# Kernel optimization log

Hardware: AMD Instinct MI355X
Metric: run time of the kernel (lower is better)

## Reference

```python
import jax, jax.numpy as jnp
import numpy as np

GROUPS = 16
GROUP_SIZE = 16
K = 3
KK = K * K
BN_EPS = 1e-5


def setup_inputs() -> dict:
    key = jax.random.key(0)
    ks = jax.random.split(key, 6)
    B, C, H, W = 16, 256, 56, 56
    mid = C // 4  # rd_ratio = 4
    x = jax.random.normal(ks[0], (B, C, H, W), dtype=jnp.float32)
    w1 = jax.random.normal(ks[1], (mid, C), dtype=jnp.float32) * (1.0 / np.sqrt(C))
    bn_gamma = jnp.ones((mid,), dtype=jnp.float32)
    bn_beta = jnp.zeros((mid,), dtype=jnp.float32)
    bn_mean = jax.random.normal(ks[2], (mid,), dtype=jnp.float32) * 0.1
    bn_var = jax.random.uniform(ks[3], (mid,), dtype=jnp.float32, minval=0.5, maxval=1.5)
    w2 = jax.random.normal(ks[4], (KK * GROUPS, mid), dtype=jnp.float32) * (1.0 / np.sqrt(mid))
    b2 = jax.random.normal(ks[5], (KK * GROUPS,), dtype=jnp.float32) * 0.01
    return {"x": x, "w1": w1, "bn_gamma": bn_gamma, "bn_beta": bn_beta,
            "bn_mean": bn_mean, "bn_var": bn_var, "w2": w2, "b2": b2}


def reference(x, w1, bn_gamma, bn_beta, bn_mean, bn_var, w2, b2):
    B, C, H, W = x.shape
    # conv1: 1x1 conv + BatchNorm (eval) + ReLU
    t = jnp.einsum('bchw,oc->bohw', x, w1)
    scale = bn_gamma / jnp.sqrt(bn_var + BN_EPS)
    t = t * scale[None, :, None, None] + (bn_beta - bn_mean * scale)[None, :, None, None]
    t = jax.nn.relu(t)
    # conv2: 1x1 conv producing per-pixel kernels (B, KK*groups, H, W)
    weight = jnp.einsum('bchw,oc->bohw', t, w2) + b2[None, :, None, None]
    weight = weight.reshape(B, GROUPS, 1, KK, H, W)
    # unfold: extract 3x3 patches (pad=1, stride=1), kernel positions row-major
    xp = jnp.pad(x, ((0, 0), (0, 0), (1, 1), (1, 1)))
    patches = jnp.stack(
        [xp[:, :, i:i + H, j:j + W] for i in range(K) for j in range(K)],
        axis=2)  # (B, C, KK, H, W), matches torch unfold's (c*KK + kk) layout
    patches = patches.reshape(B, GROUPS, GROUP_SIZE, KK, H, W)
    out = (weight * patches).sum(axis=3).reshape(B, C, H, W)
    return out
```

## Files before the change

### kernel.cpp

```cpp
#include <hip/hip_runtime.h>


#define Cn    256
#define MID   64
#define Hn    56
#define Wn    56
#define HW    3136
#define Bn    16
#define NPIX  (Bn * HW)
#define CHW   (Cn * HW)
#define NKK   9
#define NG    16
#define GSZ   16
#define PXT   64
#define BN_EPS 1e-5f

#define GLOAD_LDS(src, dst, sz)                                                        \
  __builtin_amdgcn_global_load_lds(                                                    \
      (const __attribute__((address_space(1))) void*)(src),                            \
      (__attribute__((address_space(3))) void*)(dst), (sz), 0, 0)

__global__ __launch_bounds__(256) void prep_kernel(
    const float* __restrict__ w1,
    const float* __restrict__ gamma,
    const float* __restrict__ beta,
    const float* __restrict__ mean,
    const float* __restrict__ var,
    float* __restrict__ w1f,
    float* __restrict__ bias1) {
  int idx = blockIdx.x * 256 + threadIdx.x;
  if (idx < MID * Cn) {
    int c = idx >> 6;
    int o = idx & 63;
    float scale = gamma[o] / sqrtf(var[o] + BN_EPS);
    w1f[idx] = w1[o * Cn + c] * scale;
  } else if (idx < MID * Cn + MID) {
    int o = idx - MID * Cn;
    float scale = gamma[o] / sqrtf(var[o] + BN_EPS);
    bias1[o] = beta[o] - mean[o] * scale;
  }
}

__global__ __launch_bounds__(256) void conv1_kernel(
    const float* __restrict__ x,
    const float* __restrict__ w1f,
    const float* __restrict__ bias1,
    float* __restrict__ t) {
  __shared__ __align__(16) float lx[2][16][PXT];

  const int tid = threadIdx.x;
  const int px  = tid & 63;
  const int wv  = __builtin_amdgcn_readfirstlane(tid >> 6);

  const int bid = blockIdx.x;
  const int pc  = bid >> 1;
  const int oh  = bid & 1;
  const int px0 = pc * PXT;
  const int b   = px0 / HW;
  const int hw0 = px0 - b * HW;
  const float* xb = x + (size_t)b * CHW + hw0;

  const int rsub = px >> 4;
  const int csub = (px & 15) << 2;

  GLOAD_LDS(xb + (size_t)((wv << 2) + rsub) * HW + csub, &lx[0][wv << 2][0], 16);
  __syncthreads();

  float acc[8];
#pragma unroll
  for (int j = 0; j < 8; ++j) acc[j] = 0.0f;

  for (int k = 0; k < 16; ++k) {
    const int cur = k & 1;
    if (k < 15) {
      GLOAD_LDS(xb + (size_t)((k + 1) * 16 + (wv << 2) + rsub) * HW + csub,
                &lx[cur ^ 1][wv << 2][0], 16);
    }
#pragma unroll
    for (int c = 0; c < 16; ++c) {
      const float xv = lx[cur][c][px];
      const float* wr = w1f + (((k << 4) + c) << 6) + (oh << 5) + (wv << 3);
      const float4 wa = *(const float4*)(wr + 0);
      const float4 wb = *(const float4*)(wr + 4);
      acc[0] = fmaf(xv, wa.x, acc[0]);
      acc[1] = fmaf(xv, wa.y, acc[1]);
      acc[2] = fmaf(xv, wa.z, acc[2]);
      acc[3] = fmaf(xv, wa.w, acc[3]);
      acc[4] = fmaf(xv, wb.x, acc[4]);
      acc[5] = fmaf(xv, wb.y, acc[5]);
      acc[6] = fmaf(xv, wb.z, acc[6]);
      acc[7] = fmaf(xv, wb.w, acc[7]);
    }
    __syncthreads();
  }

#pragma unroll
  for (int j = 0; j < 8; ++j) {
    const int o = (oh << 5) + (wv << 3) + j;
    t[(size_t)o * NPIX + px0 + px] = fmaxf(acc[j] + bias1[o], 0.0f);
  }
}

__global__ __launch_bounds__(256) void conv2_inv_kernel(
    const float* __restrict__ x,
    const float* __restrict__ t,
    const float* __restrict__ w2,
    const float* __restrict__ b2,
    float* __restrict__ out) {
  __shared__ __align__(16) float lt[MID][PXT];

  const int tid = threadIdx.x;
  const int px  = tid & 63;
  const int wv  = __builtin_amdgcn_readfirstlane(tid >> 6);

  const int bid = blockIdx.x;
  const int pc  = bid >> 2;
  const int gq  = bid & 3;
  const int g   = (gq << 2) + wv;

  const int px0 = pc * PXT;
  const int b   = px0 / HW;
  const int hw0 = px0 - b * HW;

  const int rsub = px >> 4;
  const int csub = (px & 15) << 2;

#pragma unroll
  for (int j = 0; j < 4; ++j) {
    const int r0 = (wv << 4) + (j << 2);
    GLOAD_LDS(t + (size_t)(r0 + rsub) * NPIX + px0 + csub, &lt[r0][0], 16);
  }
  __syncthreads();

  float a[NKK];
#pragma unroll
  for (int kk = 0; kk < NKK; ++kk) a[kk] = b2[g * NKK + kk];

  const float* wg = w2 + (size_t)g * (NKK * MID);
#pragma unroll 4
  for (int o4 = 0; o4 < MID; o4 += 4) {
    const float t0 = lt[o4 + 0][px];
    const float t1 = lt[o4 + 1][px];
    const float t2 = lt[o4 + 2][px];
    const float t3 = lt[o4 + 3][px];
#pragma unroll
    for (int kk = 0; kk < NKK; ++kk) {
      const float4 w4 = *(const float4*)(wg + (kk << 6) + o4);
      a[kk] = fmaf(t3, w4.w, fmaf(t2, w4.z, fmaf(t1, w4.y, fmaf(t0, w4.x, a[kk]))));
    }
  }

  const int hw = hw0 + px;
  const int h  = hw / Wn;
  const int w  = hw - h * Wn;

  int off[NKK];
  unsigned vmask = 0;
#pragma unroll
  for (int kk = 0; kk < NKK; ++kk) {
    const int di  = kk / 3 - 1;
    const int dj  = kk % 3 - 1;
    const int h2  = h + di;
    const int w2v = w + dj;
    const bool valid = ((unsigned)h2 < (unsigned)Hn) && ((unsigned)w2v < (unsigned)Wn);
    off[kk] = valid ? (h2 * Wn + w2v) : hw;
    vmask |= (valid ? 1u : 0u) << kk;
  }

  float wk[NKK];
#pragma unroll
  for (int kk = 0; kk < NKK; ++kk)
    wk[kk] = ((vmask >> kk) & 1u) ? a[kk] : 0.0f;

  const float* xc = x + (size_t)b * CHW + (size_t)(g * GSZ) * HW;
  float* ob = out + (size_t)b * CHW + (size_t)(g * GSZ) * HW + hw;
#pragma unroll 4
  for (int cc = 0; cc < GSZ; ++cc) {
    const float* xp = xc + (size_t)cc * HW;
    float s0 = wk[0] * xp[off[0]];
    float s1 = wk[1] * xp[off[1]];
    float s2 = wk[2] * xp[off[2]];
    s0 = fmaf(wk[3], xp[off[3]], s0);
    s1 = fmaf(wk[4], xp[off[4]], s1);
    s2 = fmaf(wk[5], xp[off[5]], s2);
    s0 = fmaf(wk[6], xp[off[6]], s0);
    s1 = fmaf(wk[7], xp[off[7]], s1);
    s2 = fmaf(wk[8], xp[off[8]], s2);
    ob[(size_t)cc * HW] = s0 + s1 + s2;
  }
}

extern "C" void kernel_launch(void* const* d_in, const int* in_sizes, int n_in,
                              void* d_out, int out_size, void* d_ws, size_t ws_size,
                              hipStream_t stream) {
  const float* x     = (const float*)d_in[0];
  const float* w1    = (const float*)d_in[1];
  const float* gamma = (const float*)d_in[2];
  const float* beta  = (const float*)d_in[3];
  const float* mean  = (const float*)d_in[4];
  const float* var   = (const float*)d_in[5];
  const float* w2    = (const float*)d_in[6];
  const float* b2    = (const float*)d_in[7];
  float* out = (float*)d_out;

  char* ws = (char*)d_ws;
  float* t     = (float*)ws;
  float* w1f   = (float*)(ws + (size_t)MID * NPIX * 4);
  float* bias1 = (float*)(ws + (size_t)MID * NPIX * 4 + (size_t)MID * Cn * 4);

  prep_kernel<<<(MID * Cn + MID + 255) / 256, 256, 0, stream>>>(
      w1, gamma, beta, mean, var, w1f, bias1);
  conv1_kernel<<<NPIX / PXT * 2, 256, 0, stream>>>(x, w1f, bias1, t);
  conv2_inv_kernel<<<NPIX / PXT * 4, 256, 0, stream>>>(x, t, w2, b2, out);
}
```

Before: 161.9 us.

## Remap conv1 to lane-per-output-channel with LDS transpose; prefetch unfold loads in conv2

conv1 now assigns one output channel per lane and 16 pixels per wave. x values are read as wave-uniform broadcast loads and w1f per lane. Results are transposed through padded LDS so t is written with float4 stores, and the grid is halved since each block covers all 64 channels. conv2 issues the first four channels' 3x3 neighbor loads before the t barrier and the conv2 matmul. It then software-pipelines the remaining channel loads against compute, reorders the block index so group quads of neighboring pixel chunks run together, and sets a minimum occupancy bound. This adds register pressure and replaces LDS-staged x in conv1 with many scalar or broadcast global loads.

Result: slower. 183.2 us (+13.1%).

```diff
diff --git a/kernel.cpp b/kernel.cpp
--- a/kernel.cpp
+++ b/kernel.cpp
@@ -46,62 +46,80 @@
     const float* __restrict__ w1f,
     const float* __restrict__ bias1,
     float* __restrict__ t) {
-  __shared__ __align__(16) float lx[2][16][PXT];
-
-  const int tid = threadIdx.x;
-  const int px  = tid & 63;
-  const int wv  = __builtin_amdgcn_readfirstlane(tid >> 6);
+  __shared__ float lt2[PXT][MID + 1];
+
+  const int tid  = threadIdx.x;
+  const int lane = tid & 63;
+  const int wv   = __builtin_amdgcn_readfirstlane(tid >> 6);
 
   const int bid = blockIdx.x;
-  const int pc  = bid >> 1;
-  const int oh  = bid & 1;
-  const int px0 = pc * PXT;
-  const int b   = px0 / HW;
-  const int hw0 = px0 - b * HW;
-  const float* xb = x + (size_t)b * CHW + hw0;
-
-  const int rsub = px >> 4;
-  const int csub = (px & 15) << 2;
-
-  GLOAD_LDS(xb + (size_t)((wv << 2) + rsub) * HW + csub, &lx[0][wv << 2][0], 16);
+  const int b   = bid / 49;
+  const int hw0 = (bid - b * 49) * PXT + wv * 16;
+  const float* xs = x + (size_t)b * CHW + hw0;
+
+  float acc[16];
+#pragma unroll
+  for (int p = 0; p < 16; ++p) acc[p] = 0.0f;
+
+  const float* wp = w1f + lane;
+
+  for (int c = 0; c < Cn; c += 4) {
+    const float w0 = wp[(c + 0) << 6];
+    const float w1 = wp[(c + 1) << 6];
+    const float w2 = wp[(c + 2) << 6];
+    const float w3 = wp[(c + 3) << 6];
+    const float* x0 = xs + (size_t)(c + 0) * HW;
+    const float* x1 = xs + (size_t)(c + 1) * HW;
+    const float* x2 = xs + (size_t)(c + 2) * HW;
+    const float* x3 = xs + (size_t)(c + 3) * HW;
+#pragma unroll
+    for (int p = 0; p < 16; ++p) acc[p] = fmaf(x0[p], w0, acc[p]);
+#pragma unroll
+    for (int p = 0; p < 16; ++p) acc[p] = fmaf(x1[p], w1, acc[p]);
+#pragma unroll
+    for (int p = 0; p < 16; ++p) acc[p] = fmaf(x2[p], w2, acc[p]);
+#pragma unroll
+    for (int p = 0; p < 16; ++p) acc[p] = fmaf(x3[p], w3, acc[p]);
+  }
+
+  const float bias = bias1[lane];
+#pragma unroll
+  for (int p = 0; p < 16; ++p)
+    lt2[wv * 16 + p][lane] = fmaxf(acc[p] + bias, 0.0f);
   __syncthreads();
 
-  float acc[8];
-#pragma unroll
-  for (int j = 0; j < 8; ++j) acc[j] = 0.0f;
-
-  for (int k = 0; k < 16; ++k) {
-    const int cur = k & 1;
-    if (k < 15) {
-      GLOAD_LDS(xb + (size_t)((k + 1) * 16 + (wv << 2) + rsub) * HW + csub,
-                &lx[cur ^ 1][wv << 2][0], 16);
-    }
-#pragma unroll
-    for (int c = 0; c < 16; ++c) {
-      const float xv = lx[cur][c][px];
-      const float* wr = w1f + (((k << 4) + c) << 6) + (oh << 5) + (wv << 3);
-      const float4 wa = *(const float4*)(wr + 0);
-      const float4 wb = *(const float4*)(wr + 4);
-      acc[0] = fmaf(xv, wa.x, acc[0]);
-      acc[1] = fmaf(xv, wa.y, acc[1]);
-      acc[2] = fmaf(xv, wa.z, acc[2]);
-      acc[3] = fmaf(xv, wa.w, acc[3]);
-      acc[4] = fmaf(xv, wb.x, acc[4]);
-      acc[5] = fmaf(xv, wb.y, acc[5]);
-      acc[6] = fmaf(xv, wb.z, acc[6]);
-      acc[7] = fmaf(xv, wb.w, acc[7]);
-    }
-    __syncthreads();
-  }
-
-#pragma unroll
-  for (int j = 0; j < 8; ++j) {
-    const int o = (oh << 5) + (wv << 3) + j;
-    t[(size_t)o * NPIX + px0 + px] = fmaxf(acc[j] + bias1[o], 0.0f);
-  }
-}
-
-__global__ __launch_bounds__(256) void conv2_inv_kernel(
+  const int orow = tid >> 2;
+  const int q    = tid & 3;
+  float v[16];
+#pragma unroll
+  for (int j = 0; j < 16; ++j) v[j] = lt2[q * 16 + j][orow];
+  float* tp = t + (size_t)orow * NPIX + bid * PXT + q * 16;
+#pragma unroll
+  for (int j = 0; j < 16; j += 4)
+    *(float4*)(tp + j) = make_float4(v[j], v[j + 1], v[j + 2], v[j + 3]);
+}
+
+#define LOADCH(dst, ch)                                                   \
+  {                                                                       \
+    const float* _xp = xcg + (size_t)(ch) * HW;                           \
+    _Pragma("unroll")                                                     \
+    for (int kk = 0; kk < NKK; ++kk) dst[kk] = _xp[off[kk]];              \
+  }
+#define CONSUME(src, ch)                                                  \
+  {                                                                       \
+    float s0 = wk[0] * src[0];                                            \
+    float s1 = wk[1] * src[1];                                            \
+    float s2 = wk[2] * src[2];                                            \
+    s0 = fmaf(wk[3], src[3], s0);                                         \
+    s1 = fmaf(wk[4], src[4], s1);                                         \
+    s2 = fmaf(wk[5], src[5], s2);                                         \
+    s0 = fmaf(wk[6], src[6], s0);                                         \
+    s1 = fmaf(wk[7], src[7], s1);                                         \
+    s2 = fmaf(wk[8], src[8], s2);                                         \
+    ob[(size_t)(ch) * HW] = s0 + s1 + s2;                                 \
+  }
+
+__global__ __launch_bounds__(256, 4) void conv2_inv_kernel(
     const float* __restrict__ x,
     const float* __restrict__ t,
     const float* __restrict__ w2,
@@ -114,8 +132,8 @@
   const int wv  = __builtin_amdgcn_readfirstlane(tid >> 6);
 
   const int bid = blockIdx.x;
-  const int pc  = bid >> 2;
-  const int gq  = bid & 3;
+  const int pc  = ((bid >> 5) << 3) + (bid & 7);
+  const int gq  = (bid >> 3) & 3;
   const int g   = (gq << 2) + wv;
 
   const int px0 = pc * PXT;
@@ -129,25 +147,6 @@
   for (int j = 0; j < 4; ++j) {
     const int r0 = (wv << 4) + (j << 2);
     GLOAD_LDS(t + (size_t)(r0 + rsub) * NPIX + px0 + csub, &lt[r0][0], 16);
-  }
-  __syncthreads();
-
-  float a[NKK];
-#pragma unroll
-  for (int kk = 0; kk < NKK; ++kk) a[kk] = b2[g * NKK + kk];
-
-  const float* wg = w2 + (size_t)g * (NKK * MID);
-#pragma unroll 4
-  for (int o4 = 0; o4 < MID; o4 += 4) {
-    const float t0 = lt[o4 + 0][px];
-    const float t1 = lt[o4 + 1][px];
-    const float t2 = lt[o4 + 2][px];
-    const float t3 = lt[o4 + 3][px];
-#pragma unroll
-    for (int kk = 0; kk < NKK; ++kk) {
-      const float4 w4 = *(const float4*)(wg + (kk << 6) + o4);
-      a[kk] = fmaf(t3, w4.w, fmaf(t2, w4.z, fmaf(t1, w4.y, fmaf(t0, w4.x, a[kk]))));
-    }
   }
 
   const int hw = hw0 + px;
@@ -167,27 +166,56 @@
     vmask |= (valid ? 1u : 0u) << kk;
   }
 
+  const float* xcg = x + (size_t)b * CHW + (size_t)(g * GSZ) * HW;
+  float p0[NKK], p1[NKK], p2[NKK], p3[NKK];
+  LOADCH(p0, 0)
+  LOADCH(p1, 1)
+  LOADCH(p2, 2)
+  LOADCH(p3, 3)
+
+  __syncthreads();
+
+  float a[NKK];
+#pragma unroll
+  for (int kk = 0; kk < NKK; ++kk) a[kk] = b2[g * NKK + kk];
+
+  const float* wg = w2 + (size_t)g * (NKK * MID);
+#pragma unroll 4
+  for (int o4 = 0; o4 < MID; o4 += 4) {
+    const float t0 = lt[o4 + 0][px];
+    const float t1 = lt[o4 + 1][px];
+    const float t2 = lt[o4 + 2][px];
+    const float t3 = lt[o4 + 3][px];
+#pragma unroll
+    for (int kk = 0; kk < NKK; ++kk) {
+      const float4 w4 = *(const float4*)(wg + (kk << 6) + o4);
+      a[kk] = fmaf(t3, w4.w, fmaf(t2, w4.z, fmaf(t1, w4.y, fmaf(t0, w4.x, a[kk]))));
+    }
+  }
+
   float wk[NKK];
 #pragma unroll
   for (int kk = 0; kk < NKK; ++kk)
     wk[kk] = ((vmask >> kk) & 1u) ? a[kk] : 0.0f;
 
-  const float* xc = x + (size_t)b * CHW + (size_t)(g * GSZ) * HW;
   float* ob = out + (size_t)b * CHW + (size_t)(g * GSZ) * HW + hw;
-#pragma unroll 4
-  for (int cc = 0; cc < GSZ; ++cc) {
-    const float* xp = xc + (size_t)cc * HW;
-    float s0 = wk[0] * xp[off[0]];
-    float s1 = wk[1] * xp[off[1]];
-    float s2 = wk[2] * xp[off[2]];
-    s0 = fmaf(wk[3], xp[off[3]], s0);
-    s1 = fmaf(wk[4], xp[off[4]], s1);
-    s2 = fmaf(wk[5], xp[off[5]], s2);
-    s0 = fmaf(wk[6], xp[off[6]], s0);
-    s1 = fmaf(wk[7], xp[off[7]], s1);
-    s2 = fmaf(wk[8], xp[off[8]], s2);
-    ob[(size_t)cc * HW] = s0 + s1 + s2;
-  }
+
+  CONSUME(p0, 0)  LOADCH(p0, 4)
+  CONSUME(p1, 1)  LOADCH(p1, 5)
+  CONSUME(p2, 2)  LOADCH(p2, 6)
+  CONSUME(p3, 3)  LOADCH(p3, 7)
+  CONSUME(p0, 4)  LOADCH(p0, 8)
+  CONSUME(p1, 5)  LOADCH(p1, 9)
+  CONSUME(p2, 6)  LOADCH(p2, 10)
+  CONSUME(p3, 7)  LOADCH(p3, 11)
+  CONSUME(p0, 8)  LOADCH(p0, 12)
+  CONSUME(p1, 9)  LOADCH(p1, 13)
+  CONSUME(p2, 10) LOADCH(p2, 14)
+  CONSUME(p3, 11) LOADCH(p3, 15)
+  CONSUME(p0, 12)
+  CONSUME(p1, 13)
+  CONSUME(p2, 14)
+  CONSUME(p3, 15)
 }
 
 extern "C" void kernel_launch(void* const* d_in, const int* in_sizes, int n_in,
@@ -210,6 +238,6 @@
 
   prep_kernel<<<(MID * Cn + MID + 255) / 256, 256, 0, stream>>>(
       w1, gamma, beta, mean, var, w1f, bias1);
-  conv1_kernel<<<NPIX / PXT * 2, 256, 0, stream>>>(x, w1f, bias1, t);
+  conv1_kernel<<<NPIX / PXT, 256, 0, stream>>>(x, w1f, bias1, t);
   conv2_inv_kernel<<<NPIX / PXT * 4, 256, 0, stream>>>(x, t, w2, b2, out);
 }
```

## Triple-buffer conv1 loads and software-pipeline x gathers in conv2 kernel

Applied to the files above, without the earlier changes.

conv1 moves from double to triple buffering of the LDS staging. It uses explicit vmcnt waits with a single barrier per iteration, so the trailing __syncthreads goes away. conv2 issues the first four channels' 3x3 gathers before the per-pixel kernel matmul and then rotates four register buffers, so global loads overlap compute. It also remaps block indices so neighbouring blocks share pixel chunks for better cache locality, and sets launch bounds for 4 blocks per CU. Register pressure rises (36 prefetch registers), which may hurt occupancy.

Result: no change. 161.1 us (-0.5%).

```diff
diff --git a/kernel.cpp b/kernel.cpp
--- a/kernel.cpp
+++ b/kernel.cpp
@@ -46,7 +46,7 @@
     const float* __restrict__ w1f,
     const float* __restrict__ bias1,
     float* __restrict__ t) {
-  __shared__ __align__(16) float lx[2][16][PXT];
+  __shared__ __align__(16) float lx[3][16][PXT];
 
   const int tid = threadIdx.x;
   const int px  = tid & 63;
@@ -62,24 +62,34 @@
 
   const int rsub = px >> 4;
   const int csub = (px & 15) << 2;
-
-  GLOAD_LDS(xb + (size_t)((wv << 2) + rsub) * HW + csub, &lx[0][wv << 2][0], 16);
-  __syncthreads();
+  const int lrow = (wv << 2) + rsub;
+
+  GLOAD_LDS(xb + (size_t)(lrow) * HW + csub, &lx[0][wv << 2][0], 16);
+  GLOAD_LDS(xb + (size_t)(16 + lrow) * HW + csub, &lx[1][wv << 2][0], 16);
 
   float acc[8];
 #pragma unroll
   for (int j = 0; j < 8; ++j) acc[j] = 0.0f;
 
   for (int k = 0; k < 16; ++k) {
-    const int cur = k & 1;
     if (k < 15) {
-      GLOAD_LDS(xb + (size_t)((k + 1) * 16 + (wv << 2) + rsub) * HW + csub,
-                &lx[cur ^ 1][wv << 2][0], 16);
-    }
+      asm volatile("s_waitcnt vmcnt(1)" ::: "memory");
+    } else {
+      asm volatile("s_waitcnt vmcnt(0)" ::: "memory");
+    }
+    __builtin_amdgcn_s_barrier();
+    __builtin_amdgcn_sched_barrier(0);
+    if (k < 14) {
+      const int nb = (k + 2) % 3;
+      GLOAD_LDS(xb + (size_t)((k + 2) * 16 + lrow) * HW + csub,
+                &lx[nb][wv << 2][0], 16);
+    }
+    const float* lxk = &lx[k % 3][0][0];
+    const float* wr0 = w1f + (k << 10) + (oh << 5) + (wv << 3);
 #pragma unroll
     for (int c = 0; c < 16; ++c) {
-      const float xv = lx[cur][c][px];
-      const float* wr = w1f + (((k << 4) + c) << 6) + (oh << 5) + (wv << 3);
+      const float xv = lxk[(c << 6) + px];
+      const float* wr = wr0 + (c << 6);
       const float4 wa = *(const float4*)(wr + 0);
       const float4 wb = *(const float4*)(wr + 4);
       acc[0] = fmaf(xv, wa.x, acc[0]);
@@ -91,7 +101,6 @@
       acc[6] = fmaf(xv, wb.z, acc[6]);
       acc[7] = fmaf(xv, wb.w, acc[7]);
     }
-    __syncthreads();
   }
 
 #pragma unroll
@@ -101,7 +110,27 @@
   }
 }
 
-__global__ __launch_bounds__(256) void conv2_inv_kernel(
+#define LOADCH(dst, ch)                                                   \
+  {                                                                       \
+    const float* _xp = xcg + (size_t)(ch) * HW;                           \
+    _Pragma("unroll")                                                     \
+    for (int kk = 0; kk < NKK; ++kk) dst[kk] = _xp[off[kk]];              \
+  }
+#define CONSUME(src, ch)                                                  \
+  {                                                                       \
+    float s0 = wk[0] * src[0];                                            \
+    float s1 = wk[1] * src[1];                                            \
+    float s2 = wk[2] * src[2];                                            \
+    s0 = fmaf(wk[3], src[3], s0);                                         \
+    s1 = fmaf(wk[4], src[4], s1);                                         \
+    s2 = fmaf(wk[5], src[5], s2);                                         \
+    s0 = fmaf(wk[6], src[6], s0);                                         \
+    s1 = fmaf(wk[7], src[7], s1);                                         \
+    s2 = fmaf(wk[8], src[8], s2);                                         \
+    ob[(size_t)(ch) * HW] = s0 + s1 + s2;                                 \
+  }
+
+__global__ __launch_bounds__(256, 4) void conv2_inv_kernel(
     const float* __restrict__ x,
     const float* __restrict__ t,
     const float* __restrict__ w2,
@@ -114,8 +143,8 @@
   const int wv  = __builtin_amdgcn_readfirstlane(tid >> 6);
 
   const int bid = blockIdx.x;
-  const int pc  = bid >> 2;
-  const int gq  = bid & 3;
+  const int pc  = ((bid >> 5) << 3) + (bid & 7);
+  const int gq  = (bid >> 3) & 3;
   const int g   = (gq << 2) + wv;
 
   const int px0 = pc * PXT;
@@ -129,25 +158,6 @@
   for (int j = 0; j < 4; ++j) {
     const int r0 = (wv << 4) + (j << 2);
     GLOAD_LDS(t + (size_t)(r0 + rsub) * NPIX + px0 + csub, &lt[r0][0], 16);
-  }
-  __syncthreads();
-
-  float a[NKK];
-#pragma unroll
-  for (int kk = 0; kk < NKK; ++kk) a[kk] = b2[g * NKK + kk];
-
-  const float* wg = w2 + (size_t)g * (NKK * MID);
-#pragma unroll 4
-  for (int o4 = 0; o4 < MID; o4 += 4) {
-    const float t0 = lt[o4 + 0][px];
-    const float t1 = lt[o4 + 1][px];
-    const float t2 = lt[o4 + 2][px];
-    const float t3 = lt[o4 + 3][px];
-#pragma unroll
-    for (int kk = 0; kk < NKK; ++kk) {
-      const float4 w4 = *(const float4*)(wg + (kk << 6) + o4);
-      a[kk] = fmaf(t3, w4.w, fmaf(t2, w4.z, fmaf(t1, w4.y, fmaf(t0, w4.x, a[kk]))));
-    }
   }
 
   const int hw = hw0 + px;
@@ -167,27 +177,56 @@
     vmask |= (valid ? 1u : 0u) << kk;
   }
 
+  const float* xcg = x + (size_t)b * CHW + (size_t)(g * GSZ) * HW;
+  float p0[NKK], p1[NKK], p2[NKK], p3[NKK];
+  LOADCH(p0, 0)
+  LOADCH(p1, 1)
+  LOADCH(p2, 2)
+  LOADCH(p3, 3)
+
+  __syncthreads();
+
+  float a[NKK];
+#pragma unroll
+  for (int kk = 0; kk < NKK; ++kk) a[kk] = b2[g * NKK + kk];
+
+  const float* wg = w2 + (size_t)g * (NKK * MID);
+#pragma unroll 4
+  for (int o4 = 0; o4 < MID; o4 += 4) {
+    const float t0 = lt[o4 + 0][px];
+    const float t1 = lt[o4 + 1][px];
+    const float t2 = lt[o4 + 2][px];
+    const float t3 = lt[o4 + 3][px];
+#pragma unroll
+    for (int kk = 0; kk < NKK; ++kk) {
+      const float4 w4 = *(const float4*)(wg + (kk << 6) + o4);
+      a[kk] = fmaf(t3, w4.w, fmaf(t2, w4.z, fmaf(t1, w4.y, fmaf(t0, w4.x, a[kk]))));
+    }
+  }
+
   float wk[NKK];
 #pragma unroll
   for (int kk = 0; kk < NKK; ++kk)
     wk[kk] = ((vmask >> kk) & 1u) ? a[kk] : 0.0f;
 
-  const float* xc = x + (size_t)b * CHW + (size_t)(g * GSZ) * HW;
   float* ob = out + (size_t)b * CHW + (size_t)(g * GSZ) * HW + hw;
-#pragma unroll 4
-  for (int cc = 0; cc < GSZ; ++cc) {
-    const float* xp = xc + (size_t)cc * HW;
-    float s0 = wk[0] * xp[off[0]];
-    float s1 = wk[1] * xp[off[1]];
-    float s2 = wk[2] * xp[off[2]];
-    s0 = fmaf(wk[3], xp[off[3]], s0);
-    s1 = fmaf(wk[4], xp[off[4]], s1);
-    s2 = fmaf(wk[5], xp[off[5]], s2);
-    s0 = fmaf(wk[6], xp[off[6]], s0);
-    s1 = fmaf(wk[7], xp[off[7]], s1);
-    s2 = fmaf(wk[8], xp[off[8]], s2);
-    ob[(size_t)cc * HW] = s0 + s1 + s2;
-  }
+
+  CONSUME(p0, 0)  LOADCH(p0, 4)
+  CONSUME(p1, 1)  LOADCH(p1, 5)
+  CONSUME(p2, 2)  LOADCH(p2, 6)
+  CONSUME(p3, 3)  LOADCH(p3, 7)
+  CONSUME(p0, 4)  LOADCH(p0, 8)
+  CONSUME(p1, 5)  LOADCH(p1, 9)
+  CONSUME(p2, 6)  LOADCH(p2, 10)
+  CONSUME(p3, 7)  LOADCH(p3, 11)
+  CONSUME(p0, 8)  LOADCH(p0, 12)
+  CONSUME(p1, 9)  LOADCH(p1, 13)
+  CONSUME(p2, 10) LOADCH(p2, 14)
+  CONSUME(p3, 11) LOADCH(p3, 15)
+  CONSUME(p0, 12)
+  CONSUME(p1, 13)
+  CONSUME(p2, 14)
+  CONSUME(p3, 15)
 }
 
 extern "C" void kernel_launch(void* const* d_in, const int* in_sizes, int n_in,
```
